# Optimization experiments

Hardware: AMD Instinct MI355X
Metric: run time of the kernel (lower is better)

Reference implementation:

```python
import jax, jax.numpy as jnp
import numpy as np


def _mlp(x, W1, b1, W2, b2):
    # Linear -> exact GELU (torch nn.GELU default) -> Linear
    h = jax.nn.gelu(x @ W1 + b1, approximate=False)
    return h @ W2 + b2


def setup_inputs() -> dict:
    B, L, H, NB, D, HID = 4, 4096, 16, 64, 1024, 128
    NS = H * NB
    key = jax.random.key(0)
    ks = jax.random.split(key, 6)
    theta_path = jax.random.normal(ks[0], (B, L, H, NB), dtype=jnp.float32)
    content_emb = jax.random.normal(ks[1], (B, L, D), dtype=jnp.float32)
    log_Pi = jnp.zeros((H, NB), dtype=jnp.float32)
    s1 = 1.0 / np.sqrt(D)
    s2 = 1.0 / np.sqrt(HID)
    # log_R_head: Linear(D,128) -> GELU -> Linear(128,NS), last weight scaled by 0.01, bias 0
    Wr1 = jax.random.uniform(ks[2], (D, HID), jnp.float32, -s1, s1)
    br1 = jnp.zeros((HID,), jnp.float32)
    Wr2 = jax.random.uniform(ks[3], (HID, NS), jnp.float32, -s2, s2) * 0.01
    br2 = jnp.zeros((NS,), jnp.float32)
    # measure_head: Linear(D,128) -> GELU -> Linear(128,NS)
    Wm1 = jax.random.uniform(ks[4], (D, HID), jnp.float32, -s1, s1)
    bm1 = jnp.zeros((HID,), jnp.float32)
    Wm2 = jax.random.uniform(ks[5], (HID, NS), jnp.float32, -s2, s2)
    bm2 = jnp.zeros((NS,), jnp.float32)
    return {
        "theta_path": theta_path, "content_emb": content_emb, "log_Pi": log_Pi,
        "Wr1": Wr1, "br1": br1, "Wr2": Wr2, "br2": br2,
        "Wm1": Wm1, "bm1": bm1, "Wm2": Wm2, "bm2": bm2,
    }


def reference(theta_path, content_emb, log_Pi, Wr1, br1, Wr2, br2, Wm1, bm1, Wm2, bm2):
    B, L, H, NB = theta_path.shape
    # per-token measurement noise R_t
    log_R = jnp.clip(_mlp(content_emb, Wr1, br1, Wr2, br2).reshape(B, L, H, NB), -5.0, 5.0)
    R = jnp.exp(log_R)
    # measurement z in (-pi, pi)
    z = jnp.pi * jnp.tanh(_mlp(content_emb, Wm1, bm1, Wm2, bm2).reshape(B, L, H, NB))
    diff = z - theta_path
    nu = jnp.arctan2(jnp.sin(diff), jnp.cos(diff))  # wrapped innovation
    Pi = jnp.exp(log_Pi)            # (H, NB) constant covariance
    Pi_b = Pi[None, None]           # (1,1,H,NB)
    K = Pi_b / jnp.maximum(Pi_b + R, 1e-8)  # Kalman gain
    alpha = 1.0 - K
    u = K * nu
    # scalar affine parallel scan: d[t] = alpha[t]*d[t-1] + u[t], d[-1]=0
    def combine(c1, c2):
        a1, v1 = c1
        a2, v2 = c2
        return a1 * a2, a2 * v1 + v2
    _, d = jax.lax.associative_scan(combine, (alpha, u), axis=1)
    theta_hat = theta_path + d
    return theta_hat, Pi, K, R
```

## Files before the change

### kernel.cpp

```cpp
#include <hip/hip_runtime.h>
#include <math.h>

static constexpr size_t OUT_THETA = 0;
static constexpr size_t OUT_PI    = 16777216;
static constexpr size_t OUT_K     = 16778240;
static constexpr size_t OUT_R     = 33555456;

#define PI_F     3.14159265358979323846f
#define INV2PI_F 0.15915494309189535f
#define PI2_HI   6.28318548202514648f
#define PI2_LO  -1.7484556e-7f
#define SPLIT_S  2048.0f
#define SPLIT_IS (1.0f / 2048.0f)

typedef _Float16 half8 __attribute__((ext_vector_type(8)));
typedef float    f32x4 __attribute__((ext_vector_type(4)));

__device__ __forceinline__ float gelu_f(float x) {
    return 0.5f * x * (1.0f + erff(x * 0.70710678118654752f));
}

__global__ __launch_bounds__(256) void k_prep(
    const float* __restrict__ Wr1, const float* __restrict__ Wm1,
    const float* __restrict__ Wr2, const float* __restrict__ Wm2,
    _Float16* __restrict__ W1rT, _Float16* __restrict__ W1mTh, _Float16* __restrict__ W1mTl,
    _Float16* __restrict__ W2rT, _Float16* __restrict__ W2mTh, _Float16* __restrict__ W2mTl)
{
    const int i = blockIdx.x * 256 + threadIdx.x;
    {
        const int k = i >> 7, c = i & 127;
        const int o = c * 1024 + k;
        W1rT[o] = (_Float16)Wr1[i];
        float w = Wm1[i];
        _Float16 h = (_Float16)w;
        W1mTh[o] = h;
        W1mTl[o] = (_Float16)((w - (float)h) * SPLIT_S);
    }
    {
        const int k = i >> 10, c = i & 1023;
        const int o = c * 128 + k;
        W2rT[o] = (_Float16)Wr2[i];
        float w = Wm2[i];
        _Float16 h = (_Float16)w;
        W2mTh[o] = h;
        W2mTl[o] = (_Float16)((w - (float)h) * SPLIT_S);
    }
}

__global__ __launch_bounds__(256, 1) void k_mm1(
    const float* __restrict__ X,
    const _Float16* __restrict__ WrT,
    const _Float16* __restrict__ WmTh, const _Float16* __restrict__ WmTl,
    const float* __restrict__ br1, const float* __restrict__ bm1,
    _Float16* __restrict__ OHr, _Float16* __restrict__ OHmh, _Float16* __restrict__ OHml)
{
    __shared__ _Float16 sm[30720];

    const int m0   = blockIdx.x * 64;
    const int tid  = threadIdx.x;
    const int lane = tid & 63;
    const int quad = lane >> 4, l15 = lane & 15;
    const int rt   = tid >> 6;

    f32x4 accR[8] = {};
    f32x4 accA[8] = {};
    f32x4 accB[8] = {};

    const float* xp = X + (size_t)(m0 + rt * 16 + l15) * 1024 + quad * 8;
    float4 xa = *(const float4*)(xp);
    float4 xb = *(const float4*)(xp + 4);

    half8 wr[2], wh[2], wl[2];
#pragma unroll
    for (int it = 0; it < 2; ++it) {
        const int u = tid + it * 256;
        const int col = u >> 2, ws = u & 3;
        const size_t go = (size_t)col * 1024 + ws * 8;
        wr[it] = *(const half8*)(WrT  + go);
        wh[it] = *(const half8*)(WmTh + go);
        wl[it] = *(const half8*)(WmTl + go);
    }
#pragma unroll
    for (int it = 0; it < 2; ++it) {
        const int u = tid + it * 256;
        const int col = u >> 2, ws = u & 3;
        *(half8*)&sm[        col * 40 + ws * 8] = wr[it];
        *(half8*)&sm[ 5120 + col * 40 + ws * 8] = wh[it];
        *(half8*)&sm[10240 + col * 40 + ws * 8] = wl[it];
    }
    __syncthreads();

    for (int k0 = 0; k0 < 1024; k0 += 32) {
        const int cur = (k0 >> 5) & 1;
        _Float16* WRc = sm + cur * 15360;
        _Float16* WHc = WRc + 5120;
        _Float16* WLc = WRc + 10240;
        const bool hasNext = (k0 + 32 < 1024);
        float4 nxa, nxb;
        if (hasNext) {
            nxa = *(const float4*)(xp + k0 + 32);
            nxb = *(const float4*)(xp + k0 + 36);
#pragma unroll
            for (int it = 0; it < 2; ++it) {
                const int u = tid + it * 256;
                const int col = u >> 2, ws = u & 3;
                const size_t go = (size_t)col * 1024 + k0 + 32 + ws * 8;
                wr[it] = *(const half8*)(WrT  + go);
                wh[it] = *(const half8*)(WmTh + go);
                wl[it] = *(const half8*)(WmTl + go);
            }
        }
        half8 ah, al;
#pragma unroll
        for (int c = 0; c < 8; ++c) {
            float v = (c < 4) ? ((const float*)&xa)[c] : ((const float*)&xb)[c - 4];
            _Float16 h = (_Float16)v;
            ah[c] = h;
            al[c] = (_Float16)((v - (float)h) * SPLIT_S);
        }
#pragma unroll
        for (int ct = 0; ct < 8; ++ct) {
            half8 bhr = *(const half8*)&WRc[(ct * 16 + l15) * 40 + quad * 8];
            accR[ct] = __builtin_amdgcn_mfma_f32_16x16x32_f16(ah, bhr, accR[ct], 0, 0, 0);
            half8 bhm = *(const half8*)&WHc[(ct * 16 + l15) * 40 + quad * 8];
            accA[ct] = __builtin_amdgcn_mfma_f32_16x16x32_f16(ah, bhm, accA[ct], 0, 0, 0);
            half8 blm = *(const half8*)&WLc[(ct * 16 + l15) * 40 + quad * 8];
            accB[ct] = __builtin_amdgcn_mfma_f32_16x16x32_f16(ah, blm, accB[ct], 0, 0, 0);
            accB[ct] = __builtin_amdgcn_mfma_f32_16x16x32_f16(al, bhm, accB[ct], 0, 0, 0);
        }
        if (hasNext) {
            _Float16* WRn = sm + (cur ^ 1) * 15360;
#pragma unroll
            for (int it = 0; it < 2; ++it) {
                const int u = tid + it * 256;
                const int col = u >> 2, ws = u & 3;
                *(half8*)&WRn[        col * 40 + ws * 8] = wr[it];
                *(half8*)&WRn[ 5120 + col * 40 + ws * 8] = wh[it];
                *(half8*)&WRn[10240 + col * 40 + ws * 8] = wl[it];
            }
            xa = nxa; xb = nxb;
        }
        __syncthreads();
    }
#pragma unroll
    for (int ct = 0; ct < 8; ++ct) {
        const int col = ct * 16 + l15;
        const float bR = br1[col];
        const float bM = bm1[col];
#pragma unroll
        for (int reg = 0; reg < 4; ++reg) {
            const int token = m0 + rt * 16 + quad * 4 + reg;
            const size_t o = (size_t)token * 128 + col;
            float gr = gelu_f(accR[ct][reg] + bR);
            OHr[o] = (_Float16)gr;
            float gm = gelu_f(accA[ct][reg] + accB[ct][reg] * SPLIT_IS + bM);
            _Float16 h = (_Float16)gm;
            OHmh[o] = h;
            OHml[o] = (_Float16)((gm - (float)h) * SPLIT_S);
        }
    }
}

__global__ __launch_bounds__(256, 4) void k_mm2(
    const _Float16* __restrict__ Hr, const _Float16* __restrict__ Hmh, const _Float16* __restrict__ Hml,
    const _Float16* __restrict__ W2rT, const _Float16* __restrict__ W2mTh, const _Float16* __restrict__ W2mTl,
    const float* __restrict__ br2, const float* __restrict__ bm2,
    const float* __restrict__ log_Pi, const float* __restrict__ theta,
    float* __restrict__ out, float* __restrict__ Aws, float* __restrict__ Uws,
    float* __restrict__ A16, float* __restrict__ U16)
{
    __shared__ _Float16 sm[15360];
    _Float16* AHr = sm;
    _Float16* AHm = sm + 2560;
    _Float16* ALm = sm + 5120;
    _Float16* BHr = sm + 7680;
    _Float16* BHm = sm + 10240;
    _Float16* BLm = sm + 12800;

    const int tt = blockIdx.x;
    const int jt = blockIdx.y;
    const int m0 = tt * 64, n0 = jt * 64;
    const int tid  = threadIdx.x;
    const int lane = tid & 63;
    const int quad = lane >> 4, l15 = lane & 15;
    const int ct   = tid >> 6;
    const int row  = tid >> 2, seg = tid & 3;

    f32x4 accr[4] = {};
    f32x4 accA[4] = {};
    f32x4 accB[4] = {};

    const size_t aobase = (size_t)(m0 + row) * 128 + seg * 8;
    const size_t bobase = (size_t)(n0 + row) * 128 + seg * 8;
    half8 la = *(const half8*)(Hr    + aobase);
    half8 lb = *(const half8*)(Hmh   + aobase);
    half8 lc = *(const half8*)(Hml   + aobase);
    half8 ld = *(const half8*)(W2rT  + bobase);
    half8 le = *(const half8*)(W2mTh + bobase);
    half8 lf = *(const half8*)(W2mTl + bobase);

    for (int k0 = 0; k0 < 128; k0 += 32) {
        __syncthreads();
        const int so = row * 40 + seg * 8;
        *(half8*)&AHr[so] = la;
        *(half8*)&AHm[so] = lb;
        *(half8*)&ALm[so] = lc;
        *(half8*)&BHr[so] = ld;
        *(half8*)&BHm[so] = le;
        *(half8*)&BLm[so] = lf;
        __syncthreads();
        if (k0 + 32 < 128) {
            la = *(const half8*)(Hr    + aobase + k0 + 32);
            lb = *(const half8*)(Hmh   + aobase + k0 + 32);
            lc = *(const half8*)(Hml   + aobase + k0 + 32);
            ld = *(const half8*)(W2rT  + bobase + k0 + 32);
            le = *(const half8*)(W2mTh + bobase + k0 + 32);
            lf = *(const half8*)(W2mTl + bobase + k0 + 32);
        }
        const int bidx = (ct * 16 + l15) * 40 + quad * 8;
        half8 br_ = *(const half8*)&BHr[bidx];
        half8 bm_ = *(const half8*)&BHm[bidx];
        half8 bl_ = *(const half8*)&BLm[bidx];
#pragma unroll
        for (int rt = 0; rt < 4; ++rt) {
            const int aidx = (rt * 16 + l15) * 40 + quad * 8;
            half8 a_r = *(const half8*)&AHr[aidx];
            half8 a_h = *(const half8*)&AHm[aidx];
            half8 a_l = *(const half8*)&ALm[aidx];
            accr[rt] = __builtin_amdgcn_mfma_f32_16x16x32_f16(a_r, br_, accr[rt], 0, 0, 0);
            accA[rt] = __builtin_amdgcn_mfma_f32_16x16x32_f16(a_h, bm_, accA[rt], 0, 0, 0);
            accB[rt] = __builtin_amdgcn_mfma_f32_16x16x32_f16(a_h, bl_, accB[rt], 0, 0, 0);
            accB[rt] = __builtin_amdgcn_mfma_f32_16x16x32_f16(a_l, bm_, accB[rt], 0, 0, 0);
        }
    }

    const int col = n0 + ct * 16 + l15;
    const float Pi_  = expf(log_Pi[col]);
    const float b2rv = br2[col];
    const float b2mv = bm2[col];
    float segA[4], segU[4];
#pragma unroll
    for (int rt = 0; rt < 4; ++rt) {
        float A = 1.0f, U = 0.0f;
#pragma unroll
        for (int reg = 0; reg < 4; ++reg) {
            const int token = m0 + rt * 16 + quad * 4 + reg;
            const size_t idx = (size_t)token * 1024 + col;
            float lr = fminf(fmaxf(accr[rt][reg] + b2rv, -5.0f), 5.0f);
            float R  = expf(lr);
            float Kg = __fdividef(Pi_, fmaxf(Pi_ + R, 1e-8f));
            float zp = accA[rt][reg] + accB[rt][reg] * SPLIT_IS + b2mv;
            float z  = PI_F * tanhf(zp);
            float d  = z - theta[idx];
            float n  = rintf(d * INV2PI_F);
            float nu = fmaf(-n, PI2_HI, d);
            nu       = fmaf(-n, PI2_LO, nu);
            float u  = Kg * nu;
            float al = 1.0f - Kg;
            U = fmaf(al, U, u);
            A *= al;
            out[OUT_K + idx]     = Kg;
            __builtin_nontemporal_store(R, &out[OUT_R + idx]);
            out[OUT_THETA + idx] = u;
        }
        segA[rt] = A; segU[rt] = U;
    }
    __syncthreads();
    float* cA = (float*)sm;
    float* cU = cA + 1088;
    const int colLocal = ct * 16 + l15;
#pragma unroll
    for (int rt = 0; rt < 4; ++rt) {
        cA[colLocal * 17 + rt * 4 + quad] = segA[rt];
        cU[colLocal * 17 + rt * 4 + quad] = segU[rt];
    }
    __syncthreads();
    if (tid < 64) {
        float A = 1.0f, U = 0.0f;
#pragma unroll
        for (int s = 0; s < 4; ++s) {
            float A4 = 1.0f, U4 = 0.0f;
#pragma unroll
            for (int q = 0; q < 4; ++q) {
                float a = cA[tid * 17 + s * 4 + q];
                float u = cU[tid * 17 + s * 4 + q];
                U4 = fmaf(a, U4, u);
                A4 *= a;
            }
            if (A16) {
                A16[((size_t)tt * 4 + s) * 1024 + n0 + tid] = A4;
                U16[((size_t)tt * 4 + s) * 1024 + n0 + tid] = U4;
            }
            U = fmaf(A4, U, U4);
            A *= A4;
        }
        Aws[(size_t)tt * 1024 + n0 + tid] = A;
        Uws[(size_t)tt * 1024 + n0 + tid] = U;
    }
}

__global__ __launch_bounds__(256) void k_carry(
    const float* __restrict__ Aws, const float* __restrict__ Uws, float* __restrict__ Cws,
    const float* __restrict__ log_Pi, float* __restrict__ out)
{
    const int b  = blockIdx.x;
    const int j4 = threadIdx.x;
    if (b == 0) {
        float4 lp = *(const float4*)(log_Pi + j4 * 4);
        float4 p;
        p.x = expf(lp.x); p.y = expf(lp.y); p.z = expf(lp.z); p.w = expf(lp.w);
        *(float4*)(out + OUT_PI + j4 * 4) = p;
    }
    float4 carry = {0.0f, 0.0f, 0.0f, 0.0f};
#pragma unroll 8
    for (int c = 0; c < 64; ++c) {
        const size_t off = (size_t)(b * 64 + c) * 1024 + j4 * 4;
        float4 a = *(const float4*)(Aws + off);
        float4 u = *(const float4*)(Uws + off);
        *(float4*)(Cws + off) = carry;
        carry.x = fmaf(a.x, carry.x, u.x);
        carry.y = fmaf(a.y, carry.y, u.y);
        carry.z = fmaf(a.z, carry.z, u.z);
        carry.w = fmaf(a.w, carry.w, u.w);
    }
}

__global__ __launch_bounds__(256) void k_apply16(
    const float* __restrict__ theta, const float* __restrict__ Cws,
    const float* __restrict__ A16, const float* __restrict__ U16,
    float* __restrict__ out)
{
    const int g   = blockIdx.x;
    const int tt  = g >> 2;
    const int cg  = g & 3;
    const int tid = threadIdx.x;
    const int s   = tid >> 6;
    const int j   = cg * 256 + (tid & 63) * 4;

    float4 d = *(const float4*)(Cws + (size_t)tt * 1024 + j);
    for (int ss = 0; ss < s; ++ss) {
        float4 a = *(const float4*)(A16 + ((size_t)tt * 4 + ss) * 1024 + j);
        float4 u = *(const float4*)(U16 + ((size_t)tt * 4 + ss) * 1024 + j);
        d.x = fmaf(a.x, d.x, u.x);
        d.y = fmaf(a.y, d.y, u.y);
        d.z = fmaf(a.z, d.z, u.z);
        d.w = fmaf(a.w, d.w, u.w);
    }
    size_t idx = (size_t)(tt * 64 + s * 16) * 1024 + j;
    const float* __restrict__ Kbase = out + OUT_K;
#pragma unroll 4
    for (int i = 0; i < 16; ++i) {
        float4 Kg = *(const float4*)(Kbase + idx);
        float4 u  = *(const float4*)(out + idx);
        float4 th = *(const float4*)(theta + idx);
        d.x = fmaf(1.0f - Kg.x, d.x, u.x);
        d.y = fmaf(1.0f - Kg.y, d.y, u.y);
        d.z = fmaf(1.0f - Kg.z, d.z, u.z);
        d.w = fmaf(1.0f - Kg.w, d.w, u.w);
        float4 r;
        r.x = th.x + d.x; r.y = th.y + d.y; r.z = th.z + d.z; r.w = th.w + d.w;
        *(float4*)(out + idx) = r;
        idx += 1024;
    }
}

__global__ __launch_bounds__(256) void k_apply(
    const float* __restrict__ theta, const float* __restrict__ Cws, float* __restrict__ out)
{
    const int bid = blockIdx.x;
    const int c   = bid & 63;
    const int b   = bid >> 6;
    const int j0  = threadIdx.x * 4;
    float4 d = *(const float4*)(Cws + (size_t)(b * 64 + c) * 1024 + j0);
    size_t idx = (size_t)(b * 4096 + c * 64) * 1024 + j0;
    const float* __restrict__ Kbase = out + OUT_K;
#pragma unroll 4
    for (int i = 0; i < 64; ++i) {
        float4 Kg = *(const float4*)(Kbase + idx);
        float4 u  = *(const float4*)(out + idx);
        float4 th = *(const float4*)(theta + idx);
        d.x = fmaf(1.0f - Kg.x, d.x, u.x);
        d.y = fmaf(1.0f - Kg.y, d.y, u.y);
        d.z = fmaf(1.0f - Kg.z, d.z, u.z);
        d.w = fmaf(1.0f - Kg.w, d.w, u.w);
        float4 r;
        r.x = th.x + d.x; r.y = th.y + d.y; r.z = th.z + d.z; r.w = th.w + d.w;
        *(float4*)(out + idx) = r;
        idx += 1024;
    }
}

extern "C" void kernel_launch(void* const* d_in, const int* in_sizes, int n_in,
                              void* d_out, int out_size, void* d_ws, size_t ws_size,
                              hipStream_t stream)
{
    const float* theta = (const float*)d_in[0];
    const float* x     = (const float*)d_in[1];
    const float* logPi = (const float*)d_in[2];
    const float* Wr1   = (const float*)d_in[3];
    const float* br1   = (const float*)d_in[4];
    const float* Wr2   = (const float*)d_in[5];
    const float* br2   = (const float*)d_in[6];
    const float* Wm1   = (const float*)d_in[7];
    const float* bm1   = (const float*)d_in[8];
    const float* Wm2   = (const float*)d_in[9];
    const float* bm2   = (const float*)d_in[10];
    float* out = (float*)d_out;

    _Float16* Hr    = (_Float16*)d_ws;
    _Float16* Hmh   = Hr  + (size_t)16384 * 128;
    _Float16* Hml   = Hmh + (size_t)16384 * 128;
    _Float16* W1rT  = Hml + (size_t)16384 * 128;
    _Float16* W1mTh = W1rT  + 131072;
    _Float16* W1mTl = W1mTh + 131072;
    _Float16* W2rT  = W1mTl + 131072;
    _Float16* W2mTh = W2rT  + 131072;
    _Float16* W2mTl = W2mTh + 131072;
    float* Aws = (float*)(W2mTl + 131072);
    float* Uws = Aws + 262144;
    float* Cws = Uws + 262144;
    float* A16 = Cws + 262144;
    float* U16 = A16 + 1048576;
    const size_t ws_need = (size_t)((char*)(U16 + 1048576) - (char*)d_ws);
    const bool seg16 = ws_size >= ws_need;

    k_prep<<<512, 256, 0, stream>>>(Wr1, Wm1, Wr2, Wm2,
                                    W1rT, W1mTh, W1mTl, W2rT, W2mTh, W2mTl);
    k_mm1<<<256, 256, 0, stream>>>(x, W1rT, W1mTh, W1mTl, br1, bm1, Hr, Hmh, Hml);
    k_mm2<<<dim3(256, 16), 256, 0, stream>>>(Hr, Hmh, Hml, W2rT, W2mTh, W2mTl,
                                             br2, bm2, logPi, theta, out, Aws, Uws,
                                             seg16 ? A16 : nullptr,
                                             seg16 ? U16 : nullptr);
    k_carry<<<4, 256, 0, stream>>>(Aws, Uws, Cws, logPi, out);
    if (seg16) {
        k_apply16<<<1024, 256, 0, stream>>>(theta, Cws, A16, U16, out);
    } else {
        k_apply<<<256, 256, 0, stream>>>(theta, Cws, out);
    }
}
```

Measured before the change: 492.7 us.

## Single-buffer mm1 LDS for occupancy, prefetch theta, use fast exp/tanh

k_mm1 drops its double-buffered LDS for a single buffer and raises its launch-bound occupancy hint to 3. Each k step now stores weights to LDS between two barriers. k_mm2 raises its occupancy hint to 5, loads all theta values up front to hide latency, and replaces expf/tanhf with __expf-based fast versions. It also changes the R store from nontemporal to a normal store. Together these trade pipelining depth and some accuracy for more concurrent blocks and cheaper transcendentals.

New measurement: 519.2 us. 1.05x slower.

```diff
diff --git a/kernel.cpp b/kernel.cpp
--- a/kernel.cpp
+++ b/kernel.cpp
@@ -18,6 +18,12 @@
 
 __device__ __forceinline__ float gelu_f(float x) {
     return 0.5f * x * (1.0f + erff(x * 0.70710678118654752f));
+}
+
+__device__ __forceinline__ float exp_fast(float x) { return __expf(x); }
+__device__ __forceinline__ float tanh_fast(float x) {
+    float e = __expf(2.0f * x);
+    return 1.0f - __fdividef(2.0f, e + 1.0f);
 }
 
 __global__ __launch_bounds__(256) void k_prep(
@@ -47,14 +53,17 @@
     }
 }
 
-__global__ __launch_bounds__(256, 1) void k_mm1(
+__global__ __launch_bounds__(256, 3) void k_mm1(
     const float* __restrict__ X,
     const _Float16* __restrict__ WrT,
     const _Float16* __restrict__ WmTh, const _Float16* __restrict__ WmTl,
     const float* __restrict__ br1, const float* __restrict__ bm1,
     _Float16* __restrict__ OHr, _Float16* __restrict__ OHmh, _Float16* __restrict__ OHml)
 {
-    __shared__ _Float16 sm[30720];
+    __shared__ _Float16 sm[15360];
+    _Float16* WR = sm;
+    _Float16* WH = sm + 5120;
+    _Float16* WL = sm + 10240;
 
     const int m0   = blockIdx.x * 64;
     const int tid  = threadIdx.x;
@@ -80,26 +89,29 @@
         wh[it] = *(const half8*)(WmTh + go);
         wl[it] = *(const half8*)(WmTl + go);
     }
-#pragma unroll
-    for (int it = 0; it < 2; ++it) {
-        const int u = tid + it * 256;
-        const int col = u >> 2, ws = u & 3;
-        *(half8*)&sm[        col * 40 + ws * 8] = wr[it];
-        *(half8*)&sm[ 5120 + col * 40 + ws * 8] = wh[it];
-        *(half8*)&sm[10240 + col * 40 + ws * 8] = wl[it];
-    }
-    __syncthreads();
 
     for (int k0 = 0; k0 < 1024; k0 += 32) {
-        const int cur = (k0 >> 5) & 1;
-        _Float16* WRc = sm + cur * 15360;
-        _Float16* WHc = WRc + 5120;
-        _Float16* WLc = WRc + 10240;
-        const bool hasNext = (k0 + 32 < 1024);
-        float4 nxa, nxb;
-        if (hasNext) {
-            nxa = *(const float4*)(xp + k0 + 32);
-            nxb = *(const float4*)(xp + k0 + 36);
+        __syncthreads();
+#pragma unroll
+        for (int it = 0; it < 2; ++it) {
+            const int u = tid + it * 256;
+            const int col = u >> 2, ws = u & 3;
+            *(half8*)&WR[col * 40 + ws * 8] = wr[it];
+            *(half8*)&WH[col * 40 + ws * 8] = wh[it];
+            *(half8*)&WL[col * 40 + ws * 8] = wl[it];
+        }
+        __syncthreads();
+        half8 ah, al;
+#pragma unroll
+        for (int c = 0; c < 8; ++c) {
+            float v = (c < 4) ? ((const float*)&xa)[c] : ((const float*)&xb)[c - 4];
+            _Float16 h = (_Float16)v;
+            ah[c] = h;
+            al[c] = (_Float16)((v - (float)h) * SPLIT_S);
+        }
+        if (k0 + 32 < 1024) {
+            xa = *(const float4*)(xp + k0 + 32);
+            xb = *(const float4*)(xp + k0 + 36);
 #pragma unroll
             for (int it = 0; it < 2; ++it) {
                 const int u = tid + it * 256;
@@ -110,37 +122,16 @@
                 wl[it] = *(const half8*)(WmTl + go);
             }
         }
-        half8 ah, al;
-#pragma unroll
-        for (int c = 0; c < 8; ++c) {
-            float v = (c < 4) ? ((const float*)&xa)[c] : ((const float*)&xb)[c - 4];
-            _Float16 h = (_Float16)v;
-            ah[c] = h;
-            al[c] = (_Float16)((v - (float)h) * SPLIT_S);
-        }
 #pragma unroll
         for (int ct = 0; ct < 8; ++ct) {
-            half8 bhr = *(const half8*)&WRc[(ct * 16 + l15) * 40 + quad * 8];
+            half8 bhr = *(const half8*)&WR[(ct * 16 + l15) * 40 + quad * 8];
             accR[ct] = __builtin_amdgcn_mfma_f32_16x16x32_f16(ah, bhr, accR[ct], 0, 0, 0);
-            half8 bhm = *(const half8*)&WHc[(ct * 16 + l15) * 40 + quad * 8];
+            half8 bhm = *(const half8*)&WH[(ct * 16 + l15) * 40 + quad * 8];
             accA[ct] = __builtin_amdgcn_mfma_f32_16x16x32_f16(ah, bhm, accA[ct], 0, 0, 0);
-            half8 blm = *(const half8*)&WLc[(ct * 16 + l15) * 40 + quad * 8];
+            half8 blm = *(const half8*)&WL[(ct * 16 + l15) * 40 + quad * 8];
             accB[ct] = __builtin_amdgcn_mfma_f32_16x16x32_f16(ah, blm, accB[ct], 0, 0, 0);
             accB[ct] = __builtin_amdgcn_mfma_f32_16x16x32_f16(al, bhm, accB[ct], 0, 0, 0);
         }
-        if (hasNext) {
-            _Float16* WRn = sm + (cur ^ 1) * 15360;
-#pragma unroll
-            for (int it = 0; it < 2; ++it) {
-                const int u = tid + it * 256;
-                const int col = u >> 2, ws = u & 3;
-                *(half8*)&WRn[        col * 40 + ws * 8] = wr[it];
-                *(half8*)&WRn[ 5120 + col * 40 + ws * 8] = wh[it];
-                *(half8*)&WRn[10240 + col * 40 + ws * 8] = wl[it];
-            }
-            xa = nxa; xb = nxb;
-        }
-        __syncthreads();
     }
 #pragma unroll
     for (int ct = 0; ct < 8; ++ct) {
@@ -161,7 +152,7 @@
     }
 }
 
-__global__ __launch_bounds__(256, 4) void k_mm2(
+__global__ __launch_bounds__(256, 5) void k_mm2(
     const _Float16* __restrict__ Hr, const _Float16* __restrict__ Hmh, const _Float16* __restrict__ Hml,
     const _Float16* __restrict__ W2rT, const _Float16* __restrict__ W2mTh, const _Float16* __restrict__ W2mTl,
     const float* __restrict__ br2, const float* __restrict__ bm2,
@@ -235,6 +226,13 @@
     }
 
     const int col = n0 + ct * 16 + l15;
+    float th[4][4];
+#pragma unroll
+    for (int rt = 0; rt < 4; ++rt)
+#pragma unroll
+        for (int reg = 0; reg < 4; ++reg)
+            th[rt][reg] = theta[(size_t)(m0 + rt * 16 + quad * 4 + reg) * 1024 + col];
+
     const float Pi_  = expf(log_Pi[col]);
     const float b2rv = br2[col];
     const float b2mv = bm2[col];
@@ -247,11 +245,11 @@
             const int token = m0 + rt * 16 + quad * 4 + reg;
             const size_t idx = (size_t)token * 1024 + col;
             float lr = fminf(fmaxf(accr[rt][reg] + b2rv, -5.0f), 5.0f);
-            float R  = expf(lr);
+            float R  = exp_fast(lr);
             float Kg = __fdividef(Pi_, fmaxf(Pi_ + R, 1e-8f));
             float zp = accA[rt][reg] + accB[rt][reg] * SPLIT_IS + b2mv;
-            float z  = PI_F * tanhf(zp);
-            float d  = z - theta[idx];
+            float z  = PI_F * tanh_fast(zp);
+            float d  = z - th[rt][reg];
             float n  = rintf(d * INV2PI_F);
             float nu = fmaf(-n, PI2_HI, d);
             nu       = fmaf(-n, PI2_LO, nu);
@@ -260,7 +258,7 @@
             U = fmaf(al, U, u);
             A *= al;
             out[OUT_K + idx]     = Kg;
-            __builtin_nontemporal_store(R, &out[OUT_R + idx]);
+            out[OUT_R + idx]     = R;
             out[OUT_THETA + idx] = u;
         }
         segA[rt] = A; segU[rt] = U;
```
